# Kernel optimization log

Hardware: AMD Instinct MI355X
Metric: run time of the kernel (lower is better)

The kernel has to match this reference:

```python
import jax, jax.numpy as jnp
import numpy as np

E = 64; H = 4; DQK = 1; B = 2; R = 1225; C = 512; EPS_LN = 1e-5


def _ln(x, g, b):
    m = x.mean(-1, keepdims=True)
    v = jnp.mean((x - m) ** 2, -1, keepdims=True)
    return (x - m) / jnp.sqrt(v + EPS_LN) * g + b


def _lin_attn(x, wq, bq, wk, bk, wv, bv, wo, bo):
    # x: (b, r, c, e); attention over axis c (nb_col), per head, ELU+1 feature map
    b_, r_, c_, e_ = x.shape
    dv = e_ // H
    q = (x @ wq.T + bq).reshape(b_, r_, c_, H, DQK).swapaxes(2, 3)  # (b,r,H,c,dqk)
    k = (x @ wk.T + bk).reshape(b_, r_, c_, H, DQK).swapaxes(2, 3)
    v = (x @ wv.T + bv).reshape(b_, r_, c_, H, dv).swapaxes(2, 3)   # (b,r,H,c,dv)
    q = jax.nn.elu(q) + 1.0
    k = jax.nn.elu(k) + 1.0
    q = q / q.mean(axis=3, keepdims=True)  # mean over seq (c)
    k = k / k.sum(axis=3, keepdims=True)   # sum over seq (c)
    ktv = jnp.einsum('brhcd,brhce->brhde', k, v)   # (b,r,H,dqk,dv)
    o = jnp.einsum('brhcd,brhde->brhce', q, ktv)   # (b,r,H,c,dv)
    o = o.swapaxes(2, 3).reshape(b_, r_, c_, e_)
    return o @ wo.T + bo


def setup_inputs():
    key = jax.random.key(0)
    ks = iter(jax.random.split(key, 32))
    def w(shape, s=0.05):
        return jax.random.normal(next(ks), shape, jnp.float32) * s
    inp = {"x": jax.random.normal(next(ks), (B, E, R, C), jnp.float32)}
    for p in ("row", "col"):
        inp[p + "_wq"] = w((H, E)); inp[p + "_bq"] = jnp.zeros((H,), jnp.float32)
        inp[p + "_wk"] = w((H, E)); inp[p + "_bk"] = jnp.zeros((H,), jnp.float32)
        inp[p + "_wv"] = w((E, E)); inp[p + "_bv"] = jnp.zeros((E,), jnp.float32)
        inp[p + "_wo"] = w((E, E)); inp[p + "_bo"] = jnp.zeros((E,), jnp.float32)
    for p in ("rn", "cn", "fn"):
        inp[p + "_g"] = jnp.ones((E,), jnp.float32)
        inp[p + "_b"] = jnp.zeros((E,), jnp.float32)
    inp["w1"] = w((4 * E, E)); inp["b1"] = jnp.zeros((4 * E,), jnp.float32)
    inp["w2"] = w((E, 4 * E)); inp["b2"] = jnp.zeros((E,), jnp.float32)
    return inp


def reference(x, row_wq, row_bq, row_wk, row_bk, row_wv, row_bv, row_wo, row_bo,
              col_wq, col_bq, col_wk, col_bk, col_wv, col_bv, col_wo, col_bo,
              rn_g, rn_b, cn_g, cn_b, fn_g, fn_b, w1, b1, w2, b2):
    xe = jnp.moveaxis(x, 1, -1)  # (B, R, C, E)
    # row attention: attend over cols (C)
    h = xe + _lin_attn(_ln(xe, rn_g, rn_b),
                       row_wq, row_bq, row_wk, row_bk, row_wv, row_bv, row_wo, row_bo)
    # col attention: attend over rows (R) -> swap axes
    hc = _ln(h.swapaxes(1, 2), cn_g, cn_b)  # (B, C, R, E)
    h = h + _lin_attn(hc, col_wq, col_bq, col_wk, col_bk, col_wv, col_bv, col_wo, col_bo).swapaxes(1, 2)
    # 1x1-conv FFN == per-position MLP with exact GELU
    f = _ln(h, fn_g, fn_b)
    f = jax.nn.gelu(f @ w1.T + b1, approximate=False) @ w2.T + b2
    return jnp.moveaxis(h + f, -1, 1)  # (B, E, R, C)
```

## Files before the change

### kernel.cpp

```cpp
#include <hip/hip_runtime.h>
#include <cmath>

#define E_ 64
#define H_ 4
#define B_ 2
#define R_ 1225
#define C_ 512
#define EPS 1e-5f

__device__ __forceinline__ float elu1(float a) { return a > 0.f ? a + 1.f : __expf(a); }

typedef float f32x4 __attribute__((ext_vector_type(4)));
typedef short bf16x8 __attribute__((ext_vector_type(8)));
typedef short bf16x4 __attribute__((ext_vector_type(4)));

__device__ __forceinline__ unsigned short f2bf(float f) {
    union { float f; unsigned u; } c; c.f = f;
    unsigned u = c.u + 0x7FFFu + ((c.u >> 16) & 1u);
    return (unsigned short)(u >> 16);
}

__device__ __forceinline__ float bf2f(unsigned short s) {
    union { unsigned u; float f; } c; c.u = ((unsigned)s) << 16;
    return c.f;
}

__device__ __forceinline__ float gelu_fast(float a) {
    const float u = a * (-1.5957691216057308f - 0.0713548162726009f * a * a);
    return a / (1.f + __expf(u));
}


#define SXR 520

__global__ __launch_bounds__(512, 2) void row_attn(
    const float* __restrict__ x,
    const float* __restrict__ wq, const float* __restrict__ bq,
    const float* __restrict__ wk, const float* __restrict__ bk,
    const float* __restrict__ wv, const float* __restrict__ bv,
    const float* __restrict__ wo, const float* __restrict__ bo,
    const float* __restrict__ lng, const float* __restrict__ lnb,
    short* __restrict__ hout)
{
    const int r = blockIdx.x;
    const int b = blockIdx.y;
    const int t = threadIdx.x;
    const int w = t >> 6;
    const int l = t & 63;
    const int lr = l & 15;
    const int lq = l >> 4;

    __shared__ short s_xT[E_][SXR];
    __shared__ short s_kb[4][SXR];
    __shared__ float s_upart[2][H_][E_];
    __shared__ float s_ktv[E_];
    __shared__ float s_wok[E_][H_];
    __shared__ float s_qm[H_];
    __shared__ float s_sk[H_];
    __shared__ float s_S1[H_];
    __shared__ float red_q[8][H_];
    __shared__ float red_k[8][H_];
    __shared__ float red_k2[8][H_];
    __shared__ float s_cst[16];

    if (t < 16) {
        const int h = t & 3;
        const int kind = t >> 2;
        const float* wm = (kind < 2) ? wq : wk;
        const float* vm = (kind & 1) ? lnb : lng;
        float acc = 0.f;
        for (int e = 0; e < E_; ++e) acc += wm[h * E_ + e] * vm[e];
        s_cst[t] = acc;
    }
    __syncthreads();

    const size_t RC = (size_t)R_ * C_;
    const float* xbase = x + (size_t)b * E_ * RC + (size_t)r * C_;

    float qs[H_];
    float aq[H_], ak[H_], ak2[H_];
    {
        const float* xp = xbase + t;
        float s = 0.f, ss = 0.f;
        float dq[H_] = {0.f, 0.f, 0.f, 0.f};
        float dk[H_] = {0.f, 0.f, 0.f, 0.f};
        #pragma unroll 16
        for (int e = 0; e < E_; ++e) {
            const float xv = xp[(size_t)e * RC];
            s += xv; ss += xv * xv;
            const float t1 = lng[e] * xv;
            #pragma unroll
            for (int h = 0; h < H_; ++h) { dq[h] += wq[h * E_ + e] * t1; dk[h] += wk[h * E_ + e] * t1; }
            s_xT[e][t] = (short)f2bf(xv);
        }
        const float mu = s * (1.f / E_);
        const float rstd = rsqrtf(ss * (1.f / E_) - mu * mu + EPS);
        const float mr = mu * rstd;
        #pragma unroll
        for (int h = 0; h < H_; ++h) {
            const float qv = elu1(rstd * dq[h] - mr * s_cst[h]     + s_cst[4 + h]  + bq[h]);
            const float kv = elu1(rstd * dk[h] - mr * s_cst[8 + h] + s_cst[12 + h] + bk[h]);
            qs[h] = qv;
            aq[h] = qv; ak[h] = kv; ak2[h] = kv * mr;
            s_kb[h][t] = (short)f2bf(kv * rstd);
        }
    }
    __syncthreads();

    {
        const int et = w & 3;
        const int kh = w >> 2;
        f32x4 uacc; uacc[0] = uacc[1] = uacc[2] = uacc[3] = 0.f;
        #pragma unroll
        for (int ks = 0; ks < 8; ++ks) {
            const int co = kh * 256 + ks * 32 + lq * 8;
            bf16x8 af;
            #pragma unroll
            for (int i = 0; i < 8; ++i) af[i] = 0;
            if (lr < 4) af = *reinterpret_cast<const bf16x8*>(&s_kb[lr][co]);
            const bf16x8 bf = *reinterpret_cast<const bf16x8*>(&s_xT[et * 16 + lr][co]);
            uacc = __builtin_amdgcn_mfma_f32_16x16x32_bf16(af, bf, uacc, 0, 0, 0);
        }
        if (lq == 0) {
            #pragma unroll
            for (int i = 0; i < 4; ++i) s_upart[kh][i][et * 16 + lr] = uacc[i];
        }
    }

    #pragma unroll
    for (int h = 0; h < H_; ++h) {
        #pragma unroll
        for (int off = 32; off; off >>= 1) {
            aq[h] += __shfl_xor(aq[h], off, 64);
            ak[h] += __shfl_xor(ak[h], off, 64);
            ak2[h] += __shfl_xor(ak2[h], off, 64);
        }
    }
    if (l == 0) {
        #pragma unroll
        for (int h = 0; h < H_; ++h) { red_q[w][h] = aq[h]; red_k[w][h] = ak[h]; red_k2[w][h] = ak2[h]; }
    }
    __syncthreads();
    if (t < H_) {
        float sq = 0.f, sk = 0.f, s1 = 0.f;
        #pragma unroll
        for (int w2 = 0; w2 < 8; ++w2) { sq += red_q[w2][t]; sk += red_k[w2][t]; s1 += red_k2[w2][t]; }
        s_qm[t] = sq * (1.f / C_);
        s_sk[t] = sk;
        s_S1[t] = s1;
    }
    __syncthreads();
    if (t < H_ * E_) {
        const int h = t >> 6, e = t & 63;
        const float m1 = s_upart[0][h][e] + s_upart[1][h][e];
        s_upart[0][h][e] = lng[e] * (m1 - s_S1[h]) + lnb[e] * s_sk[h];
    }
    __syncthreads();
    if (t < E_) {
        const int h = t >> 4;
        float acc = 0.f;
        #pragma unroll
        for (int e = 0; e < E_; ++e) acc += wv[t * E_ + e] * s_upart[0][h][e];
        s_ktv[t] = acc / s_sk[h] + bv[t];
    }
    __syncthreads();
    if (t < E_) {
        #pragma unroll
        for (int h = 0; h < H_; ++h) {
            float acc = 0.f;
            #pragma unroll
            for (int d = 0; d < 16; ++d) acc += wo[t * E_ + h * 16 + d] * s_ktv[h * 16 + d];
            s_wok[t][h] = acc;
        }
    }
    __syncthreads();

    {
        float qn[H_];
        #pragma unroll
        for (int h = 0; h < H_; ++h) qn[h] = qs[h] / s_qm[h];
        short* hp = hout + ((size_t)((size_t)b * R_ + r) * C_ + t) * E_;
        #pragma unroll
        for (int e8 = 0; e8 < 8; ++e8) {
            bf16x8 o;
            #pragma unroll
            for (int i = 0; i < 8; ++i) {
                const int e = e8 * 8 + i;
                float tt = bo[e];
                #pragma unroll
                for (int h = 0; h < H_; ++h) tt += qn[h] * s_wok[e][h];
                o[i] = (short)f2bf(bf2f((unsigned short)s_xT[e][t]) + tt);
            }
            *reinterpret_cast<bf16x8*>(hp + e8 * 8) = o;
        }
    }
}

#define SX 264

__global__ __launch_bounds__(256, 3) void col_stats(
    const short* __restrict__ hbuf,
    const float* __restrict__ wq, const float* __restrict__ bq,
    const float* __restrict__ wk, const float* __restrict__ bk,
    const float* __restrict__ wv, const float* __restrict__ bv,
    const float* __restrict__ wo,
    const float* __restrict__ lng, const float* __restrict__ lnb,
    unsigned short* __restrict__ qbuf, float* __restrict__ wokq)
{
    const int c = blockIdx.x;
    const int b = blockIdx.y;
    const int t = threadIdx.x;
    const int w = t >> 6;
    const int l = t & 63;
    const int lr = l & 15;
    const int lq = l >> 4;

    __shared__ short s_xT[E_][SX];
    __shared__ short s_kb[4][SX];
    __shared__ float s_u[H_][E_];
    __shared__ float s_ktv[E_];
    __shared__ float s_wok[E_][H_];
    __shared__ float s_qm[H_];
    __shared__ float s_sk[H_];
    __shared__ float s_S1[H_];
    __shared__ float red_q[4][H_];
    __shared__ float red_k[4][H_];
    __shared__ float red_k2[4][H_];
    __shared__ float s_cst[16];

    if (t < 16) {
        const int h = t & 3;
        const int kind = t >> 2;
        const float* wm = (kind < 2) ? wq : wk;
        const float* vm = (kind & 1) ? lnb : lng;
        float acc = 0.f;
        for (int e = 0; e < E_; ++e) acc += wm[h * E_ + e] * vm[e];
        s_cst[t] = acc;
    }
    __syncthreads();

    const size_t CE = (size_t)C_ * E_;
    const short* hp0 = hbuf + (size_t)b * R_ * CE + (size_t)c * E_;
    unsigned short* qb0 = qbuf + ((size_t)(b * C_ + c)) * R_ * 4;

    float aq[H_]  = {0.f, 0.f, 0.f, 0.f};
    float ak[H_]  = {0.f, 0.f, 0.f, 0.f};
    float ak2[H_] = {0.f, 0.f, 0.f, 0.f};
    f32x4 uacc; uacc[0] = uacc[1] = uacc[2] = uacc[3] = 0.f;

    #pragma unroll 1
    for (int it = 0; it < 5; ++it) {
        const int rr = it * 256 + t;
        if (rr < R_) {
            const short* pp = hp0 + (size_t)rr * CE;
            bf16x8 hv8[8];
            #pragma unroll
            for (int g = 0; g < 8; ++g) hv8[g] = *reinterpret_cast<const bf16x8*>(pp + g * 8);
            float s = 0.f, ss = 0.f;
            float dq[H_] = {0.f, 0.f, 0.f, 0.f};
            float dk[H_] = {0.f, 0.f, 0.f, 0.f};
            #pragma unroll
            for (int g = 0; g < 8; ++g) {
                #pragma unroll
                for (int i = 0; i < 8; ++i) {
                    const int e = g * 8 + i;
                    const float xv = bf2f((unsigned short)hv8[g][i]);
                    s += xv; ss += xv * xv;
                    const float t1 = lng[e] * xv;
                    #pragma unroll
                    for (int h = 0; h < H_; ++h) { dq[h] += wq[h * E_ + e] * t1; dk[h] += wk[h * E_ + e] * t1; }
                    s_xT[e][t] = hv8[g][i];
                }
            }
            const float mu = s * (1.f / E_);
            const float rstd = rsqrtf(ss * (1.f / E_) - mu * mu + EPS);
            const float mr = mu * rstd;
            float qv[H_];
            #pragma unroll
            for (int h = 0; h < H_; ++h) {
                qv[h] = elu1(rstd * dq[h] - mr * s_cst[h]     + s_cst[4 + h]  + bq[h]);
                const float kv = elu1(rstd * dk[h] - mr * s_cst[8 + h] + s_cst[12 + h] + bk[h]);
                aq[h] += qv[h]; ak[h] += kv; ak2[h] += kv * mr;
                s_kb[h][t] = (short)f2bf(kv * rstd);
            }
            uint2 qp;
            qp.x = ((unsigned)f2bf(qv[1]) << 16) | f2bf(qv[0]);
            qp.y = ((unsigned)f2bf(qv[3]) << 16) | f2bf(qv[2]);
            *reinterpret_cast<uint2*>(qb0 + (size_t)rr * 4) = qp;
        } else {
            #pragma unroll
            for (int e = 0; e < E_; ++e) s_xT[e][t] = 0;
            #pragma unroll
            for (int h = 0; h < H_; ++h) s_kb[h][t] = 0;
        }
        __syncthreads();
        #pragma unroll
        for (int ks = 0; ks < 8; ++ks) {
            bf16x8 af;
            #pragma unroll
            for (int i = 0; i < 8; ++i) af[i] = 0;
            if (lr < 4) af = *reinterpret_cast<const bf16x8*>(&s_kb[lr][ks * 32 + lq * 8]);
            const bf16x8 bf = *reinterpret_cast<const bf16x8*>(&s_xT[w * 16 + lr][ks * 32 + lq * 8]);
            uacc = __builtin_amdgcn_mfma_f32_16x16x32_bf16(af, bf, uacc, 0, 0, 0);
        }
        __syncthreads();
    }

    #pragma unroll
    for (int h = 0; h < H_; ++h) {
        #pragma unroll
        for (int off = 32; off; off >>= 1) {
            aq[h] += __shfl_xor(aq[h], off, 64);
            ak[h] += __shfl_xor(ak[h], off, 64);
            ak2[h] += __shfl_xor(ak2[h], off, 64);
        }
    }
    if (l == 0) {
        #pragma unroll
        for (int h = 0; h < H_; ++h) { red_q[w][h] = aq[h]; red_k[w][h] = ak[h]; red_k2[w][h] = ak2[h]; }
    }
    __syncthreads();
    if (t < H_) {
        float sq = 0.f, sk = 0.f, s1 = 0.f;
        #pragma unroll
        for (int w2 = 0; w2 < 4; ++w2) { sq += red_q[w2][t]; sk += red_k[w2][t]; s1 += red_k2[w2][t]; }
        s_qm[t] = sq * (1.f / R_);
        s_sk[t] = sk;
        s_S1[t] = s1;
    }
    __syncthreads();
    if (lq == 0) {
        const int e = w * 16 + lr;
        #pragma unroll
        for (int i = 0; i < 4; ++i)
            s_u[i][e] = lng[e] * (uacc[i] - s_S1[i]) + lnb[e] * s_sk[i];
    }
    __syncthreads();
    if (t < E_) {
        const int h = t >> 4;
        float acc = 0.f;
        #pragma unroll
        for (int e = 0; e < E_; ++e) acc += wv[t * E_ + e] * s_u[h][e];
        s_ktv[t] = acc / s_sk[h] + bv[t];
    }
    __syncthreads();
    if (t < E_) {
        #pragma unroll
        for (int h = 0; h < H_; ++h) {
            float acc = 0.f;
            #pragma unroll
            for (int d = 0; d < 16; ++d) acc += wo[t * E_ + h * 16 + d] * s_ktv[h * 16 + d];
            s_wok[t][h] = acc;
        }
    }
    __syncthreads();

    {
        const int e = t >> 2, h = t & 3;
        wokq[((size_t)(b * C_ + c)) * 256 + t] = s_wok[e][h] / s_qm[h];
    }
}

__global__ __launch_bounds__(256) void prep_weights(
    const float* __restrict__ w1, const float* __restrict__ w2,
    short* __restrict__ w1b, short* __restrict__ w2b)
{
    const int i = blockIdx.x * 256 + threadIdx.x;
    if (i < 16384) w1b[i] = (short)f2bf(w1[i]);
    else           w2b[i - 16384] = (short)f2bf(w2[i - 16384]);
}

#define SA 72
#define SG 264
#define SO 65

__global__ __launch_bounds__(256) void ffn_mfma(
    const short* __restrict__ hbuf,
    const unsigned short* __restrict__ qbuf, const float* __restrict__ wokq,
    const float* __restrict__ cbo,
    const float* __restrict__ lng, const float* __restrict__ lnb,
    const short* __restrict__ w1b, const float* __restrict__ b1,
    const short* __restrict__ w2b, const float* __restrict__ b2,
    float* __restrict__ out)
{
    __shared__ __align__(16) char smem[33792 + 16640];
    short* s_g = (short*)smem;
    short* s_a = (short*)(smem + 33792);
    float* s_o = (float*)(smem + 33792);
    float* s_ln = (float*)(smem + 43008);

    const int t = threadIdx.x;
    const int w = t >> 6;
    const int l = t & 63;
    const int lr = l & 15;
    const int lq = l >> 4;

    const int bid = blockIdx.x;
    const int cb  = bid & 7;
    const int rem = bid >> 3;
    const int r   = rem % R_;
    const int b   = rem / R_;
    const int c0  = cb * 64;

    const short* tile = hbuf + ((size_t)((size_t)b * R_ + r) * C_ + c0) * E_;

    const int m  = l;
    const int eb = w * 16;
    float hc[16];
    {
        const short* hp = tile + (size_t)m * E_ + eb;
        const bf16x8 v0 = *reinterpret_cast<const bf16x8*>(hp);
        const bf16x8 v1 = *reinterpret_cast<const bf16x8*>(hp + 8);
        const uint2 qp = *reinterpret_cast<const uint2*>(
            qbuf + ((size_t)(b * C_ + c0 + m) * R_ + r) * 4);
        float qv[4];
        qv[0] = bf2f((unsigned short)(qp.x & 0xFFFF));
        qv[1] = bf2f((unsigned short)(qp.x >> 16));
        qv[2] = bf2f((unsigned short)(qp.y & 0xFFFF));
        qv[3] = bf2f((unsigned short)(qp.y >> 16));
        const float4* wq4 = reinterpret_cast<const float4*>(
            wokq + ((size_t)(b * C_ + c0 + m)) * 256) + eb;
        float s = 0.f, ss = 0.f;
        #pragma unroll
        for (int i = 0; i < 16; ++i) {
            const int e = eb + i;
            const float4 f4 = wq4[i];
            const float hv = bf2f((unsigned short)(i < 8 ? v0[i] : v1[i - 8]));
            hc[i] = hv + cbo[e] + qv[0] * f4.x + qv[1] * f4.y + qv[2] * f4.z + qv[3] * f4.w;
            s += hc[i]; ss += hc[i] * hc[i];
        }
        s_ln[w * 64 + m]       = s;
        s_ln[256 + w * 64 + m] = ss;
    }
    __syncthreads();

    {
        const float s  = s_ln[m] + s_ln[64 + m] + s_ln[128 + m] + s_ln[192 + m];
        const float ss = s_ln[256 + m] + s_ln[320 + m] + s_ln[384 + m] + s_ln[448 + m];
        const float mu = s * (1.f / 64.f);
        const float rstd = rsqrtf(ss * (1.f / 64.f) - mu * mu + EPS);
        bf16x8 o0, o1;
        #pragma unroll
        for (int i = 0; i < 8; ++i) {
            const int e = eb + i;
            o0[i] = (short)f2bf((hc[i] - mu) * rstd * lng[e] + lnb[e]);
        }
        #pragma unroll
        for (int i = 0; i < 8; ++i) {
            const int e = eb + 8 + i;
            o1[i] = (short)f2bf((hc[8 + i] - mu) * rstd * lng[e] + lnb[e]);
        }
        *reinterpret_cast<bf16x8*>(&s_a[m * SA + eb])     = o0;
        *reinterpret_cast<bf16x8*>(&s_a[m * SA + eb + 8]) = o1;
    }
    __syncthreads();

    {
        bf16x8 bfr[4][2];
        #pragma unroll
        for (int mt = 0; mt < 4; ++mt)
            #pragma unroll
            for (int ks = 0; ks < 2; ++ks)
                bfr[mt][ks] = *reinterpret_cast<const bf16x8*>(
                    &s_a[(mt * 16 + lr) * SA + ks * 32 + lq * 8]);

        #pragma unroll
        for (int nn = 0; nn < 4; ++nn) {
            const int jt = w * 4 + nn;
            bf16x8 afr[2];
            #pragma unroll
            for (int ks = 0; ks < 2; ++ks)
                afr[ks] = *reinterpret_cast<const bf16x8*>(
                    w1b + (size_t)(jt * 16 + lr) * 64 + ks * 32 + lq * 8);
            f32x4 acc[4];
            #pragma unroll
            for (int mt = 0; mt < 4; ++mt) { acc[mt][0]=0.f; acc[mt][1]=0.f; acc[mt][2]=0.f; acc[mt][3]=0.f; }
            #pragma unroll
            for (int ks = 0; ks < 2; ++ks)
                #pragma unroll
                for (int mt = 0; mt < 4; ++mt)
                    acc[mt] = __builtin_amdgcn_mfma_f32_16x16x32_bf16(afr[ks], bfr[mt][ks], acc[mt], 0, 0, 0);

            const float4 b1v = *reinterpret_cast<const float4*>(&b1[jt * 16 + lq * 4]);
            const float* b1p = (const float*)&b1v;
            #pragma unroll
            for (int mt = 0; mt < 4; ++mt) {
                const int mm = mt * 16 + lr;
                bf16x4 pk;
                #pragma unroll
                for (int i = 0; i < 4; ++i) {
                    const float aa = acc[mt][i] + b1p[i];
                    pk[i] = (short)f2bf(gelu_fast(aa));
                }
                *reinterpret_cast<bf16x4*>(&s_g[mm * SG + jt * 16 + lq * 4]) = pk;
            }
        }
    }
    __syncthreads();

    {
        f32x4 acc2[4];
        #pragma unroll
        for (int mt = 0; mt < 4; ++mt) { acc2[mt][0]=0.f; acc2[mt][1]=0.f; acc2[mt][2]=0.f; acc2[mt][3]=0.f; }
        const int n = w * 16 + lr;
        #pragma unroll
        for (int ks = 0; ks < 8; ++ks) {
            const bf16x8 bfr = *reinterpret_cast<const bf16x8*>(
                w2b + (size_t)n * 256 + ks * 32 + lq * 8);
            #pragma unroll
            for (int mt = 0; mt < 4; ++mt) {
                const bf16x8 af = *reinterpret_cast<const bf16x8*>(
                    &s_g[(mt * 16 + lr) * SG + ks * 32 + lq * 8]);
                acc2[mt] = __builtin_amdgcn_mfma_f32_16x16x32_bf16(af, bfr, acc2[mt], 0, 0, 0);
            }
        }
        #pragma unroll
        for (int mt = 0; mt < 4; ++mt)
            #pragma unroll
            for (int i = 0; i < 4; ++i)
                s_o[(mt * 16 + lq * 4 + i) * SO + n] = acc2[mt][i];
    }
    __syncthreads();

    {
        const size_t RC = (size_t)R_ * C_;
        float* op = out + (size_t)b * E_ * RC + (size_t)r * C_ + (c0 + m);
        #pragma unroll
        for (int i = 0; i < 16; ++i) {
            const int e = eb + i;
            op[(size_t)e * RC] = hc[i] + b2[e] + s_o[m * SO + e];
        }
    }
}

extern "C" void kernel_launch(void* const* d_in, const int* in_sizes, int n_in,
                              void* d_out, int out_size, void* d_ws, size_t ws_size,
                              hipStream_t stream) {
    const float* x      = (const float*)d_in[0];
    const float* row_wq = (const float*)d_in[1];
    const float* row_bq = (const float*)d_in[2];
    const float* row_wk = (const float*)d_in[3];
    const float* row_bk = (const float*)d_in[4];
    const float* row_wv = (const float*)d_in[5];
    const float* row_bv = (const float*)d_in[6];
    const float* row_wo = (const float*)d_in[7];
    const float* row_bo = (const float*)d_in[8];
    const float* col_wq = (const float*)d_in[9];
    const float* col_bq = (const float*)d_in[10];
    const float* col_wk = (const float*)d_in[11];
    const float* col_bk = (const float*)d_in[12];
    const float* col_wv = (const float*)d_in[13];
    const float* col_bv = (const float*)d_in[14];
    const float* col_wo = (const float*)d_in[15];
    const float* col_bo = (const float*)d_in[16];
    const float* rn_g   = (const float*)d_in[17];
    const float* rn_b   = (const float*)d_in[18];
    const float* cn_g   = (const float*)d_in[19];
    const float* cn_b   = (const float*)d_in[20];
    const float* fn_g   = (const float*)d_in[21];
    const float* fn_b   = (const float*)d_in[22];
    const float* w1     = (const float*)d_in[23];
    const float* b1     = (const float*)d_in[24];
    const float* w2     = (const float*)d_in[25];
    const float* b2     = (const float*)d_in[26];

    const size_t n_h   = (size_t)B_ * R_ * C_ * E_;
    const size_t n_q   = (size_t)B_ * C_ * R_ * 4;
    const size_t n_wok = (size_t)B_ * C_ * 256;
    const size_t need  = n_h * 2 + n_q * 2 + n_wok * 4 + 2 * 16384 * 2;
    if (ws_size < need) return;

    short* hbuf = (short*)d_ws;
    unsigned short* qbuf = (unsigned short*)(hbuf + n_h);
    float* wokq = (float*)(qbuf + n_q);
    short* w1b = (short*)(wokq + n_wok);
    short* w2b = w1b + 16384;

    row_attn<<<dim3(R_, B_), 512, 0, stream>>>(
        x, row_wq, row_bq, row_wk, row_bk, row_wv, row_bv, row_wo, row_bo,
        rn_g, rn_b, hbuf);
    prep_weights<<<128, 256, 0, stream>>>(w1, w2, w1b, w2b);
    col_stats<<<dim3(C_, B_), 256, 0, stream>>>(
        hbuf, col_wq, col_bq, col_wk, col_bk, col_wv, col_bv, col_wo,
        cn_g, cn_b, qbuf, wokq);
    ffn_mfma<<<B_ * R_ * 8, 256, 0, stream>>>(
        hbuf, qbuf, wokq, col_bo, fn_g, fn_b, w1b, b1, w2b, b2, (float*)d_out);
}
```

Before: 724.1 us.

## Transpose q and wokq buffer layouts for coalesced FFN loads; vectorize output LDS reads

Stores the per-position q values as (b, r, c) instead of (b, c, r), and the wokq coefficients as (b, e, c, h) instead of (b, c, e, h). In the FFN kernel, adjacent lanes (consecutive c) then read contiguous addresses, where before they read addresses a whole stride apart. The col_stats writes become strided in exchange. The change also pads the output LDS row stride to 68 so the final readback can use float4 loads. It adds a barrier before the output tile overwrites shared memory that aliases the input tile, and switches to a cheaper bf16 rounding that does not break ties to even.

Result: faster. 630.0 us (-13.0%).

```diff
diff --git a/kernel.cpp b/kernel.cpp
--- a/kernel.cpp
+++ b/kernel.cpp
@@ -18,6 +18,11 @@
     union { float f; unsigned u; } c; c.f = f;
     unsigned u = c.u + 0x7FFFu + ((c.u >> 16) & 1u);
     return (unsigned short)(u >> 16);
+}
+
+__device__ __forceinline__ unsigned short f2bf_rn(float f) {
+    union { float f; unsigned u; } c; c.f = f;
+    return (unsigned short)((c.u + 0x8000u) >> 16);
 }
 
 __device__ __forceinline__ float bf2f(unsigned short s) {
@@ -241,7 +246,6 @@
 
     const size_t CE = (size_t)C_ * E_;
     const short* hp0 = hbuf + (size_t)b * R_ * CE + (size_t)c * E_;
-    unsigned short* qb0 = qbuf + ((size_t)(b * C_ + c)) * R_ * 4;
 
     float aq[H_]  = {0.f, 0.f, 0.f, 0.f};
     float ak[H_]  = {0.f, 0.f, 0.f, 0.f};
@@ -286,7 +290,7 @@
             uint2 qp;
             qp.x = ((unsigned)f2bf(qv[1]) << 16) | f2bf(qv[0]);
             qp.y = ((unsigned)f2bf(qv[3]) << 16) | f2bf(qv[2]);
-            *reinterpret_cast<uint2*>(qb0 + (size_t)rr * 4) = qp;
+            *reinterpret_cast<uint2*>(qbuf + (((size_t)b * R_ + rr) * C_ + c) * 4) = qp;
         } else {
             #pragma unroll
             for (int e = 0; e < E_; ++e) s_xT[e][t] = 0;
@@ -357,7 +361,7 @@
 
     {
         const int e = t >> 2, h = t & 3;
-        wokq[((size_t)(b * C_ + c)) * 256 + t] = s_wok[e][h] / s_qm[h];
+        wokq[(((size_t)b * 64 + e) * C_ + c) * 4 + h] = s_wok[e][h] / s_qm[h];
     }
 }
 
@@ -372,7 +376,7 @@
 
 #define SA 72
 #define SG 264
-#define SO 65
+#define SO 68
 
 __global__ __launch_bounds__(256) void ffn_mfma(
     const short* __restrict__ hbuf,
@@ -383,7 +387,7 @@
     const short* __restrict__ w2b, const float* __restrict__ b2,
     float* __restrict__ out)
 {
-    __shared__ __align__(16) char smem[33792 + 16640];
+    __shared__ __align__(16) char smem[51200];
     short* s_g = (short*)smem;
     short* s_a = (short*)(smem + 33792);
     float* s_o = (float*)(smem + 33792);
@@ -412,19 +416,19 @@
         const bf16x8 v0 = *reinterpret_cast<const bf16x8*>(hp);
         const bf16x8 v1 = *reinterpret_cast<const bf16x8*>(hp + 8);
         const uint2 qp = *reinterpret_cast<const uint2*>(
-            qbuf + ((size_t)(b * C_ + c0 + m) * R_ + r) * 4);
+            qbuf + (((size_t)b * R_ + r) * C_ + (c0 + m)) * 4);
         float qv[4];
         qv[0] = bf2f((unsigned short)(qp.x & 0xFFFF));
         qv[1] = bf2f((unsigned short)(qp.x >> 16));
         qv[2] = bf2f((unsigned short)(qp.y & 0xFFFF));
         qv[3] = bf2f((unsigned short)(qp.y >> 16));
-        const float4* wq4 = reinterpret_cast<const float4*>(
-            wokq + ((size_t)(b * C_ + c0 + m)) * 256) + eb;
+        const float4* wq4 = reinterpret_cast<const float4*>(wokq)
+                          + ((size_t)b * 64 + eb) * C_ + (c0 + m);
         float s = 0.f, ss = 0.f;
         #pragma unroll
         for (int i = 0; i < 16; ++i) {
             const int e = eb + i;
-            const float4 f4 = wq4[i];
+            const float4 f4 = wq4[(size_t)i * C_];
             const float hv = bf2f((unsigned short)(i < 8 ? v0[i] : v1[i - 8]));
             hc[i] = hv + cbo[e] + qv[0] * f4.x + qv[1] * f4.y + qv[2] * f4.z + qv[3] * f4.w;
             s += hc[i]; ss += hc[i] * hc[i];
@@ -443,12 +447,12 @@
         #pragma unroll
         for (int i = 0; i < 8; ++i) {
             const int e = eb + i;
-            o0[i] = (short)f2bf((hc[i] - mu) * rstd * lng[e] + lnb[e]);
+            o0[i] = (short)f2bf_rn((hc[i] - mu) * rstd * lng[e] + lnb[e]);
         }
         #pragma unroll
         for (int i = 0; i < 8; ++i) {
             const int e = eb + 8 + i;
-            o1[i] = (short)f2bf((hc[8 + i] - mu) * rstd * lng[e] + lnb[e]);
+            o1[i] = (short)f2bf_rn((hc[8 + i] - mu) * rstd * lng[e] + lnb[e]);
         }
         *reinterpret_cast<bf16x8*>(&s_a[m * SA + eb])     = o0;
         *reinterpret_cast<bf16x8*>(&s_a[m * SA + eb + 8]) = o1;
@@ -490,7 +494,7 @@
                 #pragma unroll
                 for (int i = 0; i < 4; ++i) {
                     const float aa = acc[mt][i] + b1p[i];
-                    pk[i] = (short)f2bf(gelu_fast(aa));
+                    pk[i] = (short)f2bf_rn(gelu_fast(aa));
                 }
                 *reinterpret_cast<bf16x4*>(&s_g[mm * SG + jt * 16 + lq * 4]) = pk;
             }
@@ -514,6 +518,7 @@
                 acc2[mt] = __builtin_amdgcn_mfma_f32_16x16x32_bf16(af, bfr, acc2[mt], 0, 0, 0);
             }
         }
+        __syncthreads();
         #pragma unroll
         for (int mt = 0; mt < 4; ++mt)
             #pragma unroll
@@ -526,9 +531,15 @@
         const size_t RC = (size_t)R_ * C_;
         float* op = out + (size_t)b * E_ * RC + (size_t)r * C_ + (c0 + m);
         #pragma unroll
-        for (int i = 0; i < 16; ++i) {
-            const int e = eb + i;
-            op[(size_t)e * RC] = hc[i] + b2[e] + s_o[m * SO + e];
+        for (int j = 0; j < 4; ++j) {
+            const float4 so4 = *reinterpret_cast<const float4*>(
+                &s_o[m * SO + eb + j * 4]);
+            const float* sop = (const float*)&so4;
+            #pragma unroll
+            for (int i = 0; i < 4; ++i) {
+                const int e = eb + j * 4 + i;
+                op[(size_t)e * RC] = hc[j * 4 + i] + b2[e] + sop[i];
+            }
         }
     }
 }
@@ -565,8 +576,8 @@
     const float* b2     = (const float*)d_in[26];
 
     const size_t n_h   = (size_t)B_ * R_ * C_ * E_;
-    const size_t n_q   = (size_t)B_ * C_ * R_ * 4;
-    const size_t n_wok = (size_t)B_ * C_ * 256;
+    const size_t n_q   = (size_t)B_ * R_ * C_ * 4;
+    const size_t n_wok = (size_t)B_ * 64 * C_ * 4;
     const size_t need  = n_h * 2 + n_q * 2 + n_wok * 4 + 2 * 16384 * 2;
     if (ws_size < need) return;
 
```
